# Kernel optimization log

Measured on AMD Instinct MI355X. Metric: run time of the kernel, lower is better.

## Reference

```python
import jax, jax.numpy as jnp
import numpy as np

N = 100000        # unique nodes in batch (node_num)
IN_DIM = 256
OUT_DIM = 128
E_RAND = 1_600_000  # random graph edges (avg degree 16)
B = N             # batch nodes (all nodes, each gets a self-loop edge)
SLOPE = 0.1       # leaky_relu slope_ratio


def setup_inputs() -> dict:
    key = jax.random.key(0)
    k1, k2, k3, k4, k5, k6 = jax.random.split(key, 6)
    x = jax.random.normal(k1, (N, IN_DIM), dtype=jnp.float32)
    # small weight scale keeps exp(leaky_relu(.)) in a sane range, like kaiming on unit-ish inputs
    W = jax.random.normal(k2, (OUT_DIM, IN_DIM), dtype=jnp.float32) * 0.05
    b = jax.random.normal(k3, (OUT_DIM,), dtype=jnp.float32) * 0.05
    a = jax.random.normal(k4, (2 * OUT_DIM, 1), dtype=jnp.float32) * 0.05
    src = jax.random.randint(k5, (E_RAND,), 0, N, dtype=jnp.int32)
    dst = jax.random.randint(k6, (E_RAND,), 0, N, dtype=jnp.int32)
    batch_idx = jnp.arange(B, dtype=jnp.int32)
    # append self-loop edges for every batch node (original vstacks original_node_edge)
    edges = jnp.stack([jnp.concatenate([src, batch_idx]),
                       jnp.concatenate([dst, batch_idx])], axis=1)  # [E_TOT, 2]
    return {"x": x, "W": W, "b": b, "a": a, "edges": edges, "batch_idx": batch_idx}


def reference(x, W, b, a, edges, batch_idx):
    # new_embeddings = Linear(in_dim -> out_dim)
    emb = x @ W.T + b  # [N, out_dim]
    # concat(h_src, h_dst) @ a  ==  h_src @ a[:d] + h_dst @ a[d:]
    a1 = a[:OUT_DIM, 0]
    a2 = a[OUT_DIM:, 0]
    s_src = emb @ a1  # [N]
    s_dst = emb @ a2  # [N]
    src, dst = edges[:, 0], edges[:, 1]
    logits = s_src[src] + s_dst[dst]                                 # [E]
    score = jnp.exp(jax.nn.leaky_relu(logits, negative_slope=SLOPE))  # [E]
    # sparse row-sum and aggregation fused as segment reductions over src
    row_sum = jax.ops.segment_sum(score, src, num_segments=N)        # [N]
    msgs = score[:, None] * emb[dst]                                 # [E, out_dim]
    results = jax.ops.segment_sum(msgs, src, num_segments=N)         # [N, out_dim]
    # nodes with no outgoing edges have row_sum==0; they are never gathered below
    safe_rs = jnp.where(row_sum > 0, row_sum, 1.0)
    out = results / safe_rs[:, None]
    return out[batch_idx]
```

## Files before the change

### kernel.cpp

```cpp
#include <hip/hip_runtime.h>
#include <hip/hip_fp16.h>

#define IN_DIM 256
#define OUT_DIM 128
#define SLOPE 0.1f

typedef __attribute__((ext_vector_type(8))) short short8;
typedef __attribute__((ext_vector_type(4))) float f32x4;

__device__ __forceinline__ unsigned bf16_rne(float f) {
    unsigned u = __float_as_uint(f);
    return (u + 0x7FFFu + ((u >> 16) & 1u)) >> 16;
}

__global__ __launch_bounds__(256) void wsplit_kernel(
    const float* __restrict__ W, short* __restrict__ Whi, short* __restrict__ Wlo)
{
    const int i = blockIdx.x * 256 + threadIdx.x;
    const float v = W[i];
    const unsigned hb = bf16_rne(v);
    const float hf = __uint_as_float(hb << 16);
    Whi[i] = (short)hb;
    Wlo[i] = (short)bf16_rne(v - hf);
}

__global__ __launch_bounds__(256) void gemm_rank_kernel(
    const float* __restrict__ x, const short* __restrict__ Whi_g,
    const short* __restrict__ Wlo_g, const float* __restrict__ bias,
    const float* __restrict__ a, __half* __restrict__ emb_h,
    float* __restrict__ s1, float* __restrict__ s2,
    const int* __restrict__ edges, int* __restrict__ deg,
    int* __restrict__ rank, int N, int E, int nRank)
{
    __shared__ short lds[12288];

    if ((int)blockIdx.x < nRank) {
        const int gtid   = (int)blockIdx.x * 256 + (int)threadIdx.x;
        const int stride = nRank * 256 * 4;
        int e0 = gtid * 4;
        int4 ea, eb;
        bool full = (e0 + 3 < E);
        if (full) {
            ea = ((const int4*)edges)[(e0 >> 1) + 0];
            eb = ((const int4*)edges)[(e0 >> 1) + 1];
        }
        while (e0 < E) {
            const int e0n = e0 + stride;
            int4 na, nb;
            const bool nfull = (e0n + 3 < E);
            if (nfull) {
                na = ((const int4*)edges)[(e0n >> 1) + 0];
                nb = ((const int4*)edges)[(e0n >> 1) + 1];
            }
            if (full) {
                const int r0 = atomicAdd(&deg[ea.x], 1);
                const int r1 = atomicAdd(&deg[ea.z], 1);
                const int r2 = atomicAdd(&deg[eb.x], 1);
                const int r3 = atomicAdd(&deg[eb.z], 1);
                ((int4*)rank)[e0 >> 2] = make_int4(r0, r1, r2, r3);
            } else {
                for (int e = e0; e < E; ++e) {
                    const int2 ed = ((const int2*)edges)[e];
                    rank[e] = atomicAdd(&deg[ed.x], 1);
                }
            }
            e0 = e0n; ea = na; eb = nb; full = nfull;
        }
        return;
    }

    short* Ahi = lds;
    short* Alo = lds + 2048;
    short* Bhi = lds + 4096;
    short* Blo = lds + 8192;

    const int tid = threadIdx.x;
    const int l   = tid & 63;
    const int w   = tid >> 6;
    const int gm0 = ((int)blockIdx.x - nRank) * 64;

    const int arow = tid >> 2;
    const int akc  = tid & 3;
    const int gmA  = gm0 + arow;
    const bool av_ok = (gmA < N);
    const int brow = tid >> 1;
    const int bkc0 = (tid & 1) * 2;

    f32x4 acc[8];
    #pragma unroll
    for (int j = 0; j < 8; ++j) acc[j] = (f32x4)0.f;

    float bias_v[8], av1[8], av2[8];
    #pragma unroll
    for (int nf = 0; nf < 8; ++nf) {
        const int col = nf * 16 + (l & 15);
        bias_v[nf] = bias[col];
        av1[nf]    = a[col];
        av2[nf]    = a[OUT_DIM + col];
    }

    for (int ks = 0; ks < 8; ++ks) {
        const int k0 = ks * 32;
        {
            float v[8];
            if (av_ok) {
                const float4 p0 = *(const float4*)&x[(size_t)gmA * IN_DIM + k0 + akc * 8];
                const float4 p1 = *(const float4*)&x[(size_t)gmA * IN_DIM + k0 + akc * 8 + 4];
                v[0]=p0.x; v[1]=p0.y; v[2]=p0.z; v[3]=p0.w;
                v[4]=p1.x; v[5]=p1.y; v[6]=p1.z; v[7]=p1.w;
            } else {
                #pragma unroll
                for (int j = 0; j < 8; ++j) v[j] = 0.f;
            }
            short8 h8, l8;
            #pragma unroll
            for (int j = 0; j < 8; ++j) {
                unsigned hb = bf16_rne(v[j]);
                float hf = __uint_as_float(hb << 16);
                h8[j] = (short)hb;
                l8[j] = (short)bf16_rne(v[j] - hf);
            }
            *(short8*)&Ahi[akc * 512 + arow * 8] = h8;
            *(short8*)&Alo[akc * 512 + arow * 8] = l8;
        }
        #pragma unroll
        for (int q = 0; q < 2; ++q) {
            const int kc = bkc0 + q;
            const short8 h8 = *(const short8*)&Whi_g[brow * IN_DIM + k0 + kc * 8];
            const short8 l8 = *(const short8*)&Wlo_g[brow * IN_DIM + k0 + kc * 8];
            *(short8*)&Bhi[kc * 1024 + brow * 8] = h8;
            *(short8*)&Blo[kc * 1024 + brow * 8] = l8;
        }
        __syncthreads();

        const int arow_f = w * 16 + (l & 15);
        const int aoff   = (l >> 4) * 512 + arow_f * 8;
        const short8 ah = *(const short8*)&Ahi[aoff];
        const short8 al = *(const short8*)&Alo[aoff];
        #pragma unroll
        for (int nf = 0; nf < 8; ++nf) {
            const int col = nf * 16 + (l & 15);
            const int boff = (l >> 4) * 1024 + col * 8;
            const short8 bh = *(const short8*)&Bhi[boff];
            const short8 bl = *(const short8*)&Blo[boff];
            acc[nf] = __builtin_amdgcn_mfma_f32_16x16x32_bf16(ah, bh, acc[nf], 0, 0, 0);
            acc[nf] = __builtin_amdgcn_mfma_f32_16x16x32_bf16(al, bh, acc[nf], 0, 0, 0);
            acc[nf] = __builtin_amdgcn_mfma_f32_16x16x32_bf16(ah, bl, acc[nf], 0, 0, 0);
        }
        __syncthreads();
    }

    __half* hl = (__half*)lds;
    #pragma unroll
    for (int r = 0; r < 4; ++r) {
        const int lrow = w * 16 + (l >> 4) * 4 + r;
        float p1 = 0.f, p2 = 0.f;
        #pragma unroll
        for (int nf = 0; nf < 8; ++nf) {
            const float e = acc[nf][r] + bias_v[nf];
            p1 += e * av1[nf];
            p2 += e * av2[nf];
            hl[lrow * 144 + nf * 16 + (l & 15)] = __float2half(e);
        }
        p1 += __shfl_xor(p1, 1); p1 += __shfl_xor(p1, 2);
        p1 += __shfl_xor(p1, 4); p1 += __shfl_xor(p1, 8);
        p2 += __shfl_xor(p2, 1); p2 += __shfl_xor(p2, 2);
        p2 += __shfl_xor(p2, 4); p2 += __shfl_xor(p2, 8);
        const int gm = gm0 + lrow;
        if ((l & 15) == 0 && gm < N) { s1[gm] = p1; s2[gm] = p2; }
    }
    __syncthreads();
    #pragma unroll
    for (int i = 0; i < 4; ++i) {
        const int idx = i * 256 + tid;
        const int row = idx >> 4, seg = idx & 15;
        if (gm0 + row < N) {
            const uint4 u = *(const uint4*)&hl[row * 144 + seg * 8];
            ((uint4*)emb_h)[(size_t)(gm0 + row) * 16 + seg] = u;
        }
    }
}

__global__ __launch_bounds__(256) void scan1_kernel(
    const int* __restrict__ deg, int* __restrict__ off,
    int* __restrict__ bsum, int N)
{
    __shared__ int lds[256];
    const int t = threadIdx.x;
    const int base = blockIdx.x * 1024 + t * 4;
    int v[4];
    int ts = 0;
    #pragma unroll
    for (int j = 0; j < 4; ++j) {
        v[j] = (base + j < N) ? deg[base + j] : 0;
        ts += v[j];
    }
    lds[t] = ts;
    __syncthreads();
    for (int d = 1; d < 256; d <<= 1) {
        int xv = (t >= d) ? lds[t - d] : 0;
        __syncthreads();
        lds[t] += xv;
        __syncthreads();
    }
    int run = lds[t] - ts;
    #pragma unroll
    for (int j = 0; j < 4; ++j) {
        if (base + j < N) off[base + j] = run;
        run += v[j];
    }
    if (t == 255) bsum[blockIdx.x] = lds[255];
}

__global__ __launch_bounds__(256) void scan3_kernel(
    int* __restrict__ off, const int* __restrict__ bsum,
    const int* __restrict__ bidx, int* __restrict__ flag, int N, int E)
{
    __shared__ int red[256];
    const int t = threadIdx.x;
    const int chunk = (int)(blockIdx.x >> 2);
    int s = 0;
    for (int j = t; j < chunk; j += 256) s += bsum[j];
    red[t] = s;
    __syncthreads();
    #pragma unroll
    for (int d = 128; d > 0; d >>= 1) {
        if (t < d) red[t] += red[t + d];
        __syncthreads();
    }
    const int pref = red[0];
    const int i = blockIdx.x * 256 + t;
    if (i < N) {
        off[i] += pref;
        if (bidx[i] != i) atomicOr(flag, 1);
    }
    if (i == 0) off[N] = E;
}

__global__ __launch_bounds__(256) void fill_kernel(
    const int* __restrict__ edges, const int* __restrict__ off,
    const int* __restrict__ rank, int* __restrict__ csr, int E)
{
    const int e0 = (blockIdx.x * 256 + threadIdx.x) * 4;
    if (e0 + 3 < E) {
        const int4 ea = ((const int4*)edges)[(e0 >> 1) + 0];
        const int4 eb = ((const int4*)edges)[(e0 >> 1) + 1];
        const int4 rk = ((const int4*)rank)[e0 >> 2];
        csr[off[ea.x] + rk.x] = ea.y;
        csr[off[ea.z] + rk.y] = ea.w;
        csr[off[eb.x] + rk.z] = eb.y;
        csr[off[eb.z] + rk.w] = eb.w;
    } else if (e0 < E) {
        for (int e = e0; e < E; ++e) {
            const int2 ed = ((const int2*)edges)[e];
            csr[off[ed.x] + rank[e]] = ed.y;
        }
    }
}

__global__ __launch_bounds__(256) void agg_kernel(
    const int* __restrict__ off, const int* __restrict__ csr,
    const float* __restrict__ s1, const float* __restrict__ s2,
    const __half* __restrict__ emb_h, const int* __restrict__ flag,
    float* __restrict__ results, float* __restrict__ out, int N)
{
    __shared__ int2 sl[4][64];

    const int wid  = (int)((blockIdx.x * 256u + threadIdx.x) >> 6);
    const int lane = threadIdx.x & 63;
    const int wv   = threadIdx.x >> 6;
    if (wid >= N) return;
    const int eg = lane >> 4;
    const int cl = lane & 15;
    const int beg = off[wid];
    const int end = off[wid + 1];
    const float s1n = s1[wid];

    const float4* __restrict__ embrow = (const float4*)emb_h;
    int2* slot = &sl[wv][0];

    float av[8];
    #pragma unroll
    for (int k = 0; k < 8; ++k) av[k] = 0.f;
    float rsl = 0.f;

    for (int tile = beg; tile < end; tile += 64) {
        const int cnt = min(64, end - tile);
        int d = 0; float sc = 0.f;
        if (lane < cnt) {
            d = csr[tile + lane];
            const float ll = s1n + s2[d];
            sc = __expf(ll > 0.f ? ll : SLOPE * ll);
        }
        rsl += sc;
        slot[lane] = make_int2(d, __float_as_int(sc));
        __builtin_amdgcn_wave_barrier();
        for (int j0 = 0; j0 < cnt; j0 += 32) {
            const int nq = ((cnt - j0) + 3) >> 2;
            int dq[8]; float scq[8];
            #pragma unroll
            for (int q = 0; q < 8; ++q) {
                dq[q] = 0; scq[q] = 0.f;
                if (q < nq) {
                    const int2 p = slot[j0 + q * 4 + eg];
                    dq[q] = p.x; scq[q] = __int_as_float(p.y);
                }
            }
            float4 vq[8];
            #pragma unroll
            for (int q = 0; q < 8; ++q)
                if (q < nq) vq[q] = embrow[(size_t)dq[q] * 16 + cl];
            #pragma unroll
            for (int q = 0; q < 8; ++q) {
                if (q < nq) {
                    const __half* hp = reinterpret_cast<const __half*>(&vq[q]);
                    #pragma unroll
                    for (int k = 0; k < 8; ++k)
                        av[k] += scq[q] * __half2float(hp[k]);
                }
            }
        }
        __builtin_amdgcn_wave_barrier();
    }

    float rs = rsl;
    rs += __shfl_xor(rs, 1);  rs += __shfl_xor(rs, 2);
    rs += __shfl_xor(rs, 4);  rs += __shfl_xor(rs, 8);
    rs += __shfl_xor(rs, 16); rs += __shfl_xor(rs, 32);
    #pragma unroll
    for (int k = 0; k < 8; ++k) {
        av[k] += __shfl_xor(av[k], 16);
        av[k] += __shfl_xor(av[k], 32);
    }

    const float inv = 1.f / (rs > 0.f ? rs : 1.f);
    if (eg == 0) {
        float* dbuf = (*flag == 0) ? out : results;
        float4* rp = (float4*)&dbuf[(size_t)wid * 128 + cl * 8];
        rp[0] = make_float4(av[0] * inv, av[1] * inv, av[2] * inv, av[3] * inv);
        rp[1] = make_float4(av[4] * inv, av[5] * inv, av[6] * inv, av[7] * inv);
    }
}

__global__ __launch_bounds__(256) void gather_kernel(
    const float* __restrict__ results, const int* __restrict__ bidx,
    const int* __restrict__ flag, float* __restrict__ out, int N)
{
    if (*flag == 0) return;
    const unsigned i = blockIdx.x * 256u + threadIdx.x;
    if (i >= (unsigned)N * 32u) return;
    const unsigned n = i >> 5, c = i & 31;
    ((float4*)out)[i] = ((const float4*)results)[(size_t)bidx[n] * 32 + c];
}

extern "C" void kernel_launch(void* const* d_in, const int* in_sizes, int n_in,
                              void* d_out, int out_size, void* d_ws, size_t ws_size,
                              hipStream_t stream) {
    const float* x     = (const float*)d_in[0];
    const float* W     = (const float*)d_in[1];
    const float* b     = (const float*)d_in[2];
    const float* a     = (const float*)d_in[3];
    const int*   edges = (const int*)d_in[4];
    const int*   bidx  = (const int*)d_in[5];

    const int N = in_sizes[5];
    const int E = in_sizes[4] / 2;

    float*  results = (float*)d_ws;
    __half* emb_h   = (__half*)(results + (size_t)N * OUT_DIM);
    int*    rank    = (int*)(emb_h + (size_t)N * OUT_DIM);
    int*    csr     = rank + E;
    float*  s1      = (float*)(csr + E);
    float*  s2      = s1 + N;
    int*    deg     = (int*)(s2 + N);
    int*    flag    = deg + N;
    int*    off     = flag + 1;
    int*    bsum    = off + N + 1;
    short*  Whi     = (short*)(bsum + 256);
    short*  Wlo     = Whi + OUT_DIM * IN_DIM;

    hipMemsetAsync(deg, 0, (size_t)(N + 1) * sizeof(int), stream);

    wsplit_kernel<<<(OUT_DIM * IN_DIM) / 256, 256, 0, stream>>>(W, Whi, Wlo);

    const int nRank = 128;
    const int nGemm = (N + 63) / 64;
    gemm_rank_kernel<<<nRank + nGemm, 256, 0, stream>>>(
        x, Whi, Wlo, b, a, emb_h, s1, s2, edges, deg, rank, N, E, nRank);

    const int nb = (N + 1023) / 1024;
    scan1_kernel<<<nb, 256, 0, stream>>>(deg, off, bsum, N);
    scan3_kernel<<<(N + 255) / 256, 256, 0, stream>>>(off, bsum, bidx, flag, N, E);

    const int gE4 = (E / 4 + 255) / 256 + 1;
    fill_kernel<<<gE4, 256, 0, stream>>>(edges, off, rank, csr, E);

    const unsigned aggThreads = (unsigned)N * 64u;
    agg_kernel<<<(aggThreads + 255u) / 256u, 256, 0, stream>>>(
        off, csr, s1, s2, emb_h, flag, results, (float*)d_out, N);

    const unsigned gatherThreads = (unsigned)N * 32u;
    gather_kernel<<<(gatherThreads + 255u) / 256u, 256, 0, stream>>>(
        results, bidx, flag, (float*)d_out, N);
}
```

Before: 193.6 us.

## Split degree counters into four replicas to reduce atomic contention

Rank-assignment atomics now go into one of four replicated degree arrays, picked by thread index, instead of a single counter array. The scan sums the four replicas, and a new interleaved per-node offset table (off4) holds each replica's starting position, so the fill kernel scatters edges without collisions. The aim is to spread same-address atomic traffic and cut serialization in the degree-counting phase. The cost is four times the memset and counter memory, extra reads in the scan, and a new off4 table that scan3 writes and fill reads.

```diff
diff --git a/kernel.cpp b/kernel.cpp
--- a/kernel.cpp
+++ b/kernel.cpp
@@ -29,7 +29,7 @@
     const short* __restrict__ Wlo_g, const float* __restrict__ bias,
     const float* __restrict__ a, __half* __restrict__ emb_h,
     float* __restrict__ s1, float* __restrict__ s2,
-    const int* __restrict__ edges, int* __restrict__ deg,
+    const int* __restrict__ edges, int* __restrict__ deg4,
     int* __restrict__ rank, int N, int E, int nRank)
 {
     __shared__ short lds[12288];
@@ -37,6 +37,7 @@
     if ((int)blockIdx.x < nRank) {
         const int gtid   = (int)blockIdx.x * 256 + (int)threadIdx.x;
         const int stride = nRank * 256 * 4;
+        int* __restrict__ degr = deg4 + (size_t)(gtid & 3) * N;
         int e0 = gtid * 4;
         int4 ea, eb;
         bool full = (e0 + 3 < E);
@@ -53,15 +54,15 @@
                 nb = ((const int4*)edges)[(e0n >> 1) + 1];
             }
             if (full) {
-                const int r0 = atomicAdd(&deg[ea.x], 1);
-                const int r1 = atomicAdd(&deg[ea.z], 1);
-                const int r2 = atomicAdd(&deg[eb.x], 1);
-                const int r3 = atomicAdd(&deg[eb.z], 1);
+                const int r0 = atomicAdd(&degr[ea.x], 1);
+                const int r1 = atomicAdd(&degr[ea.z], 1);
+                const int r2 = atomicAdd(&degr[eb.x], 1);
+                const int r3 = atomicAdd(&degr[eb.z], 1);
                 ((int4*)rank)[e0 >> 2] = make_int4(r0, r1, r2, r3);
             } else {
                 for (int e = e0; e < E; ++e) {
                     const int2 ed = ((const int2*)edges)[e];
-                    rank[e] = atomicAdd(&deg[ed.x], 1);
+                    rank[e] = atomicAdd(&degr[ed.x], 1);
                 }
             }
             e0 = e0n; ea = na; eb = nb; full = nfull;
@@ -182,7 +183,7 @@
 }
 
 __global__ __launch_bounds__(256) void scan1_kernel(
-    const int* __restrict__ deg, int* __restrict__ off,
+    const int* __restrict__ deg4, int* __restrict__ off,
     int* __restrict__ bsum, int N)
 {
     __shared__ int lds[256];
@@ -192,7 +193,10 @@
     int ts = 0;
     #pragma unroll
     for (int j = 0; j < 4; ++j) {
-        v[j] = (base + j < N) ? deg[base + j] : 0;
+        const int idx = base + j;
+        v[j] = 0;
+        if (idx < N)
+            v[j] = deg4[idx] + deg4[N + idx] + deg4[2 * N + idx] + deg4[3 * N + idx];
         ts += v[j];
     }
     lds[t] = ts;
@@ -214,6 +218,7 @@
 
 __global__ __launch_bounds__(256) void scan3_kernel(
     int* __restrict__ off, const int* __restrict__ bsum,
+    const int* __restrict__ deg4, int* __restrict__ off4,
     const int* __restrict__ bidx, int* __restrict__ flag, int N, int E)
 {
     __shared__ int red[256];
@@ -231,29 +236,33 @@
     const int pref = red[0];
     const int i = blockIdx.x * 256 + t;
     if (i < N) {
-        off[i] += pref;
+        const int o = off[i] + pref;
+        off[i] = o;
+        const int c0 = deg4[i], c1 = deg4[N + i], c2 = deg4[2 * N + i];
+        ((int4*)off4)[i] = make_int4(o, o + c0, o + c0 + c1, o + c0 + c1 + c2);
         if (bidx[i] != i) atomicOr(flag, 1);
     }
     if (i == 0) off[N] = E;
 }
 
 __global__ __launch_bounds__(256) void fill_kernel(
-    const int* __restrict__ edges, const int* __restrict__ off,
+    const int* __restrict__ edges, const int* __restrict__ off4,
     const int* __restrict__ rank, int* __restrict__ csr, int E)
 {
     const int e0 = (blockIdx.x * 256 + threadIdx.x) * 4;
+    const int r  = (e0 >> 2) & 3;
     if (e0 + 3 < E) {
         const int4 ea = ((const int4*)edges)[(e0 >> 1) + 0];
         const int4 eb = ((const int4*)edges)[(e0 >> 1) + 1];
         const int4 rk = ((const int4*)rank)[e0 >> 2];
-        csr[off[ea.x] + rk.x] = ea.y;
-        csr[off[ea.z] + rk.y] = ea.w;
-        csr[off[eb.x] + rk.z] = eb.y;
-        csr[off[eb.z] + rk.w] = eb.w;
+        csr[off4[4 * ea.x + r] + rk.x] = ea.y;
+        csr[off4[4 * ea.z + r] + rk.y] = ea.w;
+        csr[off4[4 * eb.x + r] + rk.z] = eb.y;
+        csr[off4[4 * eb.z + r] + rk.w] = eb.w;
     } else if (e0 < E) {
         for (int e = e0; e < E; ++e) {
             const int2 ed = ((const int2*)edges)[e];
-            csr[off[ed.x] + rank[e]] = ed.y;
+            csr[off4[4 * ed.x + r] + rank[e]] = ed.y;
         }
     }
 }
@@ -372,28 +381,30 @@
     int*    csr     = rank + E;
     float*  s1      = (float*)(csr + E);
     float*  s2      = s1 + N;
-    int*    deg     = (int*)(s2 + N);
-    int*    flag    = deg + N;
-    int*    off     = flag + 1;
-    int*    bsum    = off + N + 1;
+    int*    deg4    = (int*)(s2 + N);
+    int*    flag    = deg4 + 4 * (size_t)N;
+    int*    off     = flag + 4;
+    int*    off4    = off + N + 4;
+    int*    bsum    = off4 + 4 * (size_t)N;
     short*  Whi     = (short*)(bsum + 256);
     short*  Wlo     = Whi + OUT_DIM * IN_DIM;
 
-    hipMemsetAsync(deg, 0, (size_t)(N + 1) * sizeof(int), stream);
+    hipMemsetAsync(deg4, 0, (size_t)(4 * (size_t)N + 4) * sizeof(int), stream);
 
     wsplit_kernel<<<(OUT_DIM * IN_DIM) / 256, 256, 0, stream>>>(W, Whi, Wlo);
 
     const int nRank = 128;
     const int nGemm = (N + 63) / 64;
     gemm_rank_kernel<<<nRank + nGemm, 256, 0, stream>>>(
-        x, Whi, Wlo, b, a, emb_h, s1, s2, edges, deg, rank, N, E, nRank);
+        x, Whi, Wlo, b, a, emb_h, s1, s2, edges, deg4, rank, N, E, nRank);
 
     const int nb = (N + 1023) / 1024;
-    scan1_kernel<<<nb, 256, 0, stream>>>(deg, off, bsum, N);
-    scan3_kernel<<<(N + 255) / 256, 256, 0, stream>>>(off, bsum, bidx, flag, N, E);
+    scan1_kernel<<<nb, 256, 0, stream>>>(deg4, off, bsum, N);
+    scan3_kernel<<<(N + 255) / 256, 256, 0, stream>>>(
+        off, bsum, deg4, off4, bidx, flag, N, E);
 
     const int gE4 = (E / 4 + 255) / 256 + 1;
-    fill_kernel<<<gE4, 256, 0, stream>>>(edges, off, rank, csr, E);
+    fill_kernel<<<gE4, 256, 0, stream>>>(edges, off4, rank, csr, E);
 
     const unsigned aggThreads = (unsigned)N * 64u;
     agg_kernel<<<(aggThreads + 255u) / 256u, 256, 0, stream>>>(
```

New measurement: 197.9 us. 2.3% more time.
